# Optimization experiments

Hardware: AMD Instinct MI355X
Metric: run time of the kernel (lower is better)

The kernel has to match this reference:

```python
import jax, jax.numpy as jnp
import numpy as np

N_NODES = 100000
N_EDGES = 640000
D_IN = 128
D_OUT = 128


def setup_inputs() -> dict:
    key = jax.random.key(0)
    k1, k2, k3, k4 = jax.random.split(key, 4)
    x = jax.random.normal(k1, (N_NODES, D_IN), dtype=jnp.float32)
    edge_index = jax.random.randint(k2, (2, N_EDGES), 0, N_NODES, dtype=jnp.int64)
    # nn.Linear(input_dim, out_dim): weight [out, in], bias [out]
    bound = 1.0 / np.sqrt(D_IN)
    W = jax.random.uniform(k3, (D_OUT, D_IN), minval=-bound, maxval=bound, dtype=jnp.float32)
    b = jax.random.uniform(k4, (D_OUT,), minval=-bound, maxval=bound, dtype=jnp.float32)
    return {"x": x, "edge_index": edge_index, "W": W, "b": b}


def reference(x, edge_index, W, b):
    # GINConv (eps=0): h_i = (1+eps)*x_i + sum_{j in N(i)} x_j, then Linear(h)
    src = edge_index[0]
    dst = edge_index[1]
    agg = jax.ops.segment_sum(x[src], dst, num_segments=N_NODES)  # [N, D_IN]
    h = x + agg
    return h @ W.T + b  # [N, D_OUT]
```

## Files before the change

kernel.cpp:

```cpp
#include <hip/hip_runtime.h>
#include <hip/hip_bf16.h>

#define N_NODES 100000
#define N_EDGES 640000
#define D 128
#define NBINS 782
#define NBINSP 784
#define CHB 320
#define CHE 2000
#define CAP 2048
#define GB 1563
#define TB (GB + CHB)
#define ZROW N_NODES
#define CSRN (NBINS * 128)

typedef __attribute__((ext_vector_type(8))) short short8;
typedef __attribute__((ext_vector_type(4))) float f32x4;

__device__ __forceinline__ short f32_to_bf16(float f) {
  union { float f; unsigned u; } c; c.f = f;
  unsigned u = c.u;
  unsigned r = (u + 0x7FFFu + ((u >> 16) & 1u)) >> 16;
  return (short)r;
}
__device__ __forceinline__ float lo_bf16(unsigned v) {
  union { unsigned u; float f; } c; c.u = v << 16; return c.f;
}
__device__ __forceinline__ float hi_bf16(unsigned v) {
  union { unsigned u; float f; } c; c.u = v & 0xFFFF0000u; return c.f;
}

__global__ __launch_bounds__(256) void gemm_count(const float* x, const float* W,
                                                  const int* ei, short* y, int* hist) {
  __shared__ char ldsbuf[128 * 136 * 2];
  int b = blockIdx.x;
  int g_incl = ((b + 1) * GB) / TB;
  bool is_gemm = g_incl > (b * GB) / TB;
  int t = threadIdx.x;

  if (!is_gemm) {
    int* h = (int*)ldsbuf;
    int sid = b - g_incl;
    for (int j = t; j < NBINSP; j += 256) h[j] = 0;
    __syncthreads();
    int base = sid * CHE;
    for (int i = t; i < CHE; i += 256) {
      int dst = ei[N_EDGES + base + i];
      atomicAdd(&h[dst >> 7], 1);
    }
    __syncthreads();
    for (int j = t; j < NBINSP; j += 256) hist[sid * NBINSP + j] = h[j];
    return;
  }

  short (*Wlds)[136] = (short(*)[136])ldsbuf;
  int gb = g_incl - 1;
  for (int idx = t * 8; idx < D * D; idx += 256 * 8) {
    int r = idx >> 7, c = idx & 127;
    float4 a = *reinterpret_cast<const float4*>(W + idx);
    float4 bb = *reinterpret_cast<const float4*>(W + idx + 4);
    short8 s;
    s[0] = f32_to_bf16(a.x);  s[1] = f32_to_bf16(a.y);
    s[2] = f32_to_bf16(a.z);  s[3] = f32_to_bf16(a.w);
    s[4] = f32_to_bf16(bb.x); s[5] = f32_to_bf16(bb.y);
    s[6] = f32_to_bf16(bb.z); s[7] = f32_to_bf16(bb.w);
    *reinterpret_cast<short8*>(&Wlds[r][c]) = s;
  }
  __syncthreads();

  int wave = t >> 6, lane = t & 63;
  int l15 = lane & 15, kq = lane >> 4;
  int row0 = gb * 64 + wave * 16;
  if (row0 >= N_NODES) return;
  int ar = row0 + l15;
  if (ar >= N_NODES) ar = N_NODES - 1;
  const float* xrow = x + (size_t)ar * D;

  f32x4 acc[8];
#pragma unroll
  for (int n = 0; n < 8; ++n) acc[n] = (f32x4){0.f, 0.f, 0.f, 0.f};

#pragma unroll
  for (int kk = 0; kk < 4; ++kk) {
    int k0 = kk * 32 + kq * 8;
    float4 a0 = *reinterpret_cast<const float4*>(xrow + k0);
    float4 a1 = *reinterpret_cast<const float4*>(xrow + k0 + 4);
    short8 af;
    af[0] = f32_to_bf16(a0.x); af[1] = f32_to_bf16(a0.y);
    af[2] = f32_to_bf16(a0.z); af[3] = f32_to_bf16(a0.w);
    af[4] = f32_to_bf16(a1.x); af[5] = f32_to_bf16(a1.y);
    af[6] = f32_to_bf16(a1.z); af[7] = f32_to_bf16(a1.w);
#pragma unroll
    for (int n = 0; n < 8; ++n) {
      short8 bf = *reinterpret_cast<short8*>(&Wlds[n * 16 + l15][k0]);
      acc[n] = __builtin_amdgcn_mfma_f32_16x16x32_bf16(af, bf, acc[n], 0, 0, 0);
    }
  }

  int orow0 = row0 + kq * 4;
#pragma unroll
  for (int n = 0; n < 8; ++n) {
#pragma unroll
    for (int r = 0; r < 4; ++r) {
      int row = orow0 + r;
      if (row < N_NODES)
        y[(size_t)row * D + n * 16 + l15] = f32_to_bf16(acc[n][r]);
    }
  }
}

__global__ __launch_bounds__(256) void scan_cols(const int* hist, int* scanned, int* bintot) {
  __shared__ int sdata[256];
  int j = blockIdx.x;
  int t = threadIdx.x;
  int a = 0, b = 0;
  if (t < CHB / 2) {
    a = hist[(2 * t) * NBINSP + j];
    b = hist[(2 * t + 1) * NBINSP + j];
  }
  int ps = a + b;
  sdata[t] = ps;
  __syncthreads();
  int incl = ps;
  for (int off = 1; off < 256; off <<= 1) {
    int u = (t >= off) ? sdata[t - off] : 0;
    __syncthreads();
    incl += u;
    sdata[t] = incl;
    __syncthreads();
  }
  if (t < CHB / 2) {
    int excl = incl - ps;
    scanned[j * CHB + 2 * t] = excl;
    scanned[j * CHB + 2 * t + 1] = excl + a;
  }
  if (t == CHB / 2 - 1) bintot[j] = incl;
}

__global__ __launch_bounds__(256) void scan_bins(const int* bintot, int* bases, short* y) {
  __shared__ int sdata[256];
  int t = threadIdx.x;
  if (t < 64) ((int*)(y + (size_t)ZROW * D))[t] = 0;

  int v0 = 0, v1 = 0, v2 = 0, v3 = 0;
  if (t < NBINSP / 4) {
    int4 vv = *reinterpret_cast<const int4*>(bintot + 4 * t);
    v0 = vv.x; v1 = vv.y; v2 = vv.z; v3 = vv.w;
  }
  int s = v0 + v1 + v2 + v3;
  sdata[t] = s;
  __syncthreads();
  int incl = s;
  for (int off = 1; off < 256; off <<= 1) {
    int u = (t >= off) ? sdata[t - off] : 0;
    __syncthreads();
    incl += u;
    sdata[t] = incl;
    __syncthreads();
  }
  if (t < NBINSP / 4) {
    int e = incl - s;
    bases[4 * t + 0] = e;
    bases[4 * t + 1] = e + v0;
    bases[4 * t + 2] = e + v0 + v1;
    bases[4 * t + 3] = e + v0 + v1 + v2;
  }
  if (t == NBINSP / 4 - 1) bases[NBINSP] = incl;
}

__global__ __launch_bounds__(256) void bin_place(const int* ei, const int* scanned,
                                                 const int* bases, int* binned) {
  __shared__ int rk[NBINSP];
  __shared__ int cb[NBINSP];
  int t = threadIdx.x, b = blockIdx.x;
  for (int j = t; j < NBINSP; j += 256) {
    rk[j] = 0;
    cb[j] = bases[j] + scanned[j * CHB + b];
  }
  __syncthreads();
  int base = b * CHE;
  for (int i = t; i < CHE; i += 256) {
    int e = base + i;
    int src = ei[e];
    int dst = ei[N_EDGES + e];
    int bin = dst >> 7;
    int r = atomicAdd(&rk[bin], 1);
    binned[cb[bin] + r] = ((dst & 127) << 17) | src;
  }
}

__global__ __launch_bounds__(256) void sort_bins32(const int* binned, const int* bases,
                                                   int* csr32, int* ndeg) {
  __shared__ int c[128];
  int bin = blockIdx.x, t = threadIdx.x;
  if (t < 128) c[t] = 0;
  __syncthreads();
  int est = bases[bin];
  int E = bases[bin + 1] - est;
  if (E > CAP) E = CAP;

#pragma unroll
  for (int j = 0; j < 8; ++j) {
    int i = j * 256 + t;
    if (i < E) {
      int p = binned[est + i];
      int off = p >> 17;
      int r = atomicAdd(&c[off], 1);
      if (r < 32)
        csr32[(size_t)((bin << 7) + off) * 32 + r] = p & 0x1FFFF;
    }
  }
  __syncthreads();

  if (t < 128) {
    int gnode = (bin << 7) + t;
    if (gnode < N_NODES) ndeg[gnode] = c[t];
  }
  for (int s = t; s < 128 * 32; s += 256) {
    int node = s >> 5, slot = s & 31;
    if (slot >= c[node])
      csr32[(size_t)((bin << 7) + node) * 32 + slot] = ZROW;
  }
}

__global__ __launch_bounds__(256) void gather32(const short* y, const int* ndeg,
                                                const int* csr32, const float* bias,
                                                float* out) {
  int gtid = blockIdx.x * 256 + threadIdx.x;
  int wave = gtid >> 6;
  int lane = threadIdx.x & 63;
  int g = lane >> 5;
  int l = lane & 31;
  int node = wave * 2 + g;

  int deg = ndeg[node];
  if (deg > 32) deg = 32;
  int dother = __shfl_xor(deg, 32);
  int kmaxw = deg > dother ? deg : dother;

  int ids = csr32[(size_t)node * 32 + l];
  int base_sl = lane & 32;

  const uint2* yq = (const uint2*)y;
  uint2 self = yq[(size_t)node * 32 + l];

  float4 acc[8];
#pragma unroll
  for (int i = 0; i < 8; ++i) acc[i] = make_float4(0.f, 0.f, 0.f, 0.f);

  for (int k = 0; k < kmaxw; k += 8) {
#pragma unroll
    for (int i = 0; i < 8; ++i) {
      int src = __shfl(ids, base_sl + k + i);
      uint2 w = yq[(size_t)src * 32 + l];
      acc[i].x += lo_bf16(w.x);
      acc[i].y += hi_bf16(w.x);
      acc[i].z += lo_bf16(w.y);
      acc[i].w += hi_bf16(w.y);
    }
  }

  float4 bv = ((const float4*)bias)[l];
  float4 tot;
  tot.x = (lo_bf16(self.x) + bv.x) + (((acc[0].x + acc[1].x) + (acc[2].x + acc[3].x)) +
                                      ((acc[4].x + acc[5].x) + (acc[6].x + acc[7].x)));
  tot.y = (hi_bf16(self.x) + bv.y) + (((acc[0].y + acc[1].y) + (acc[2].y + acc[3].y)) +
                                      ((acc[4].y + acc[5].y) + (acc[6].y + acc[7].y)));
  tot.z = (lo_bf16(self.y) + bv.z) + (((acc[0].z + acc[1].z) + (acc[2].z + acc[3].z)) +
                                      ((acc[4].z + acc[5].z) + (acc[6].z + acc[7].z)));
  tot.w = (hi_bf16(self.y) + bv.w) + (((acc[0].w + acc[1].w) + (acc[2].w + acc[3].w)) +
                                      ((acc[4].w + acc[5].w) + (acc[6].w + acc[7].w)));

  ((float4*)out)[(size_t)node * 32 + l] = tot;
}

__global__ void copy_x(const float4* x, float4* h, int n4) {
  int i = blockIdx.x * blockDim.x + threadIdx.x;
  int s = gridDim.x * blockDim.x;
  for (; i < n4; i += s) h[i] = x[i];
}

__global__ void scatter_add(const float* x, const int* ei, float* h) {
  int i = blockIdx.x * blockDim.x + threadIdx.x;
  int s = gridDim.x * blockDim.x;
  const int total = N_EDGES * 32;
  for (; i < total; i += s) {
    int e = i >> 5;
    int c = (i & 31) << 2;
    int src = ei[e];
    int dst = ei[N_EDGES + e];
    float4 v = *reinterpret_cast<const float4*>(x + (size_t)src * D + c);
    float* hp = h + (size_t)dst * D + c;
    unsafeAtomicAdd(hp + 0, v.x);
    unsafeAtomicAdd(hp + 1, v.y);
    unsafeAtomicAdd(hp + 2, v.z);
    unsafeAtomicAdd(hp + 3, v.w);
  }
}

__global__ __launch_bounds__(256) void gin_gemm_f32(const float* h, const float* W,
                                                    const float* bias, float* out) {
  __shared__ short Wlds[128][136];
  int t = threadIdx.x;
  for (int idx = t * 8; idx < D * D; idx += 256 * 8) {
    int r = idx >> 7, c = idx & 127;
    float4 a = *reinterpret_cast<const float4*>(W + idx);
    float4 b = *reinterpret_cast<const float4*>(W + idx + 4);
    short8 s;
    s[0] = f32_to_bf16(a.x); s[1] = f32_to_bf16(a.y);
    s[2] = f32_to_bf16(a.z); s[3] = f32_to_bf16(a.w);
    s[4] = f32_to_bf16(b.x); s[5] = f32_to_bf16(b.y);
    s[6] = f32_to_bf16(b.z); s[7] = f32_to_bf16(b.w);
    *reinterpret_cast<short8*>(&Wlds[r][c]) = s;
  }
  __syncthreads();

  int wave = t >> 6, lane = t & 63;
  int l15 = lane & 15, kq = lane >> 4;
  int row0 = blockIdx.x * 64 + wave * 16;
  if (row0 >= N_NODES) return;
  int ar = row0 + l15;
  if (ar >= N_NODES) ar = N_NODES - 1;
  const float* hrow = h + (size_t)ar * D;

  f32x4 acc[8];
#pragma unroll
  for (int n = 0; n < 8; ++n) acc[n] = (f32x4){0.f, 0.f, 0.f, 0.f};

#pragma unroll
  for (int kk = 0; kk < 4; ++kk) {
    int k0 = kk * 32 + kq * 8;
    float4 a0 = *reinterpret_cast<const float4*>(hrow + k0);
    float4 a1 = *reinterpret_cast<const float4*>(hrow + k0 + 4);
    short8 af;
    af[0] = f32_to_bf16(a0.x); af[1] = f32_to_bf16(a0.y);
    af[2] = f32_to_bf16(a0.z); af[3] = f32_to_bf16(a0.w);
    af[4] = f32_to_bf16(a1.x); af[5] = f32_to_bf16(a1.y);
    af[6] = f32_to_bf16(a1.z); af[7] = f32_to_bf16(a1.w);
#pragma unroll
    for (int n = 0; n < 8; ++n) {
      short8 bf = *reinterpret_cast<short8*>(&Wlds[n * 16 + l15][k0]);
      acc[n] = __builtin_amdgcn_mfma_f32_16x16x32_bf16(af, bf, acc[n], 0, 0, 0);
    }
  }

  int orow0 = row0 + kq * 4;
#pragma unroll
  for (int n = 0; n < 8; ++n) {
    float bv = bias[n * 16 + l15];
#pragma unroll
    for (int r = 0; r < 4; ++r) {
      int row = orow0 + r;
      if (row < N_NODES)
        out[(size_t)row * D + n * 16 + l15] = acc[n][r] + bv;
    }
  }
}

extern "C" void kernel_launch(void* const* d_in, const int* in_sizes, int n_in,
                              void* d_out, int out_size, void* d_ws, size_t ws_size,
                              hipStream_t stream) {
  const float* x   = (const float*)d_in[0];
  const int*   ei  = (const int*)d_in[1];
  const float* W   = (const float*)d_in[2];
  const float* bia = (const float*)d_in[3];
  float* out = (float*)d_out;
  (void)in_sizes; (void)n_in; (void)out_size;

  const size_t HIST_I   = (size_t)CHB * NBINSP;
  const size_t SCAN_I   = (size_t)NBINSP * CHB;
  const size_t BINTOT_I = NBINSP;
  const size_t BASES_I  = 800;
  const size_t BINNED_I = N_EDGES;
  const size_t CSR_I    = (size_t)CSRN * 32;
  const size_t NDG_I    = CSRN;
  const size_t INTS = HIST_I + SCAN_I + BINTOT_I + BASES_I + BINNED_I + CSR_I + NDG_I;
  const size_t Y_B  = (size_t)(N_NODES + 1) * D * 2;
  const size_t NEED = INTS * 4 + Y_B;

  if (ws_size >= NEED) {
    int* hist    = (int*)d_ws;
    int* scanned = hist + HIST_I;
    int* bintot  = scanned + SCAN_I;
    int* bases   = bintot + BINTOT_I;
    int* binned  = bases + BASES_I;
    int* csr32   = binned + BINNED_I;
    int* ndeg    = csr32 + CSR_I;
    short* y     = (short*)(ndeg + NDG_I);

    gemm_count <<<TB, 256, 0, stream>>>(x, W, ei, y, hist);
    scan_cols  <<<NBINSP, 256, 0, stream>>>(hist, scanned, bintot);
    scan_bins  <<<1, 256, 0, stream>>>(bintot, bases, y);
    bin_place  <<<CHB, 256, 0, stream>>>(ei, scanned, bases, binned);
    sort_bins32<<<NBINS, 256, 0, stream>>>(binned, bases, csr32, ndeg);
    gather32   <<<(N_NODES / 2) / 4, 256, 0, stream>>>(y, ndeg, csr32, bia, out);
  } else {
    int n4 = N_NODES * D / 4;
    copy_x<<<(n4 + 255) / 256, 256, 0, stream>>>((const float4*)x, (float4*)out, n4);
    int total = N_EDGES * 32;
    scatter_add<<<(total + 255) / 256, 256, 0, stream>>>(x, ei, out);
    gin_gemm_f32<<<(N_NODES + 63) / 64, 256, 0, stream>>>(out, W, bia, out);
  }
}
```

Before: 92.17 us.

## Split GEMM across place and sort kernels, use nontemporal memory ops

```diff
diff --git a/kernel.cpp b/kernel.cpp
--- a/kernel.cpp
+++ b/kernel.cpp
@@ -9,8 +9,9 @@
 #define CHB 320
 #define CHE 2000
 #define CAP 2048
-#define GB 1563
-#define TB (GB + CHB)
+#define GBT 1563
+#define GA 400
+#define GB2 (GBT - GA)
 #define ZROW N_NODES
 #define CSRN (NBINS * 128)
 
@@ -30,31 +31,10 @@
   union { unsigned u; float f; } c; c.u = v & 0xFFFF0000u; return c.f;
 }
 
-__global__ __launch_bounds__(256) void gemm_count(const float* x, const float* W,
-                                                  const int* ei, short* y, int* hist) {
-  __shared__ char ldsbuf[128 * 136 * 2];
-  int b = blockIdx.x;
-  int g_incl = ((b + 1) * GB) / TB;
-  bool is_gemm = g_incl > (b * GB) / TB;
-  int t = threadIdx.x;
-
-  if (!is_gemm) {
-    int* h = (int*)ldsbuf;
-    int sid = b - g_incl;
-    for (int j = t; j < NBINSP; j += 256) h[j] = 0;
-    __syncthreads();
-    int base = sid * CHE;
-    for (int i = t; i < CHE; i += 256) {
-      int dst = ei[N_EDGES + base + i];
-      atomicAdd(&h[dst >> 7], 1);
-    }
-    __syncthreads();
-    for (int j = t; j < NBINSP; j += 256) hist[sid * NBINSP + j] = h[j];
-    return;
-  }
-
+__device__ __forceinline__ void gemm_body(const float* x, const float* W, short* y,
+                                          int gb, char* ldsbuf) {
   short (*Wlds)[136] = (short(*)[136])ldsbuf;
-  int gb = g_incl - 1;
+  int t = threadIdx.x;
   for (int idx = t * 8; idx < D * D; idx += 256 * 8) {
     int r = idx >> 7, c = idx & 127;
     float4 a = *reinterpret_cast<const float4*>(W + idx);
@@ -109,6 +89,27 @@
   }
 }
 
+#define HETERO_MAP(S_, G_)                                   \
+  int b = blockIdx.x;                                        \
+  int g_incl = ((b + 1) * (G_)) / ((S_) + (G_));             \
+  bool is_gemm = g_incl > (b * (G_)) / ((S_) + (G_));        \
+  int sid = b - g_incl;                                      \
+  int gb_loc = g_incl - 1;
+
+__global__ __launch_bounds__(256) void bin_count(const int* ei, int* hist) {
+  __shared__ int h[NBINSP];
+  int t = threadIdx.x, b = blockIdx.x;
+  for (int j = t; j < NBINSP; j += 256) h[j] = 0;
+  __syncthreads();
+  int base = b * CHE;
+  for (int i = t; i < CHE; i += 256) {
+    int dst = ei[N_EDGES + base + i];
+    atomicAdd(&h[dst >> 7], 1);
+  }
+  __syncthreads();
+  for (int j = t; j < NBINSP; j += 256) hist[b * NBINSP + j] = h[j];
+}
+
 __global__ __launch_bounds__(256) void scan_cols(const int* hist, int* scanned, int* bintot) {
   __shared__ int sdata[256];
   int j = blockIdx.x;
@@ -168,31 +169,44 @@
   if (t == NBINSP / 4 - 1) bases[NBINSP] = incl;
 }
 
-__global__ __launch_bounds__(256) void bin_place(const int* ei, const int* scanned,
-                                                 const int* bases, int* binned) {
-  __shared__ int rk[NBINSP];
-  __shared__ int cb[NBINSP];
-  int t = threadIdx.x, b = blockIdx.x;
+__global__ __launch_bounds__(256) void p4_place_gemm(const float* x, const float* W,
+                                                     short* y, const int* ei,
+                                                     const int* scanned, const int* bases,
+                                                     int* binned) {
+  __shared__ char ldsbuf[34816];
+  HETERO_MAP(CHB, GA)
+  int t = threadIdx.x;
+  if (is_gemm) { gemm_body(x, W, y, gb_loc, ldsbuf); return; }
+
+  int* rk = (int*)ldsbuf;
+  int* cb = rk + NBINSP;
   for (int j = t; j < NBINSP; j += 256) {
     rk[j] = 0;
-    cb[j] = bases[j] + scanned[j * CHB + b];
-  }
-  __syncthreads();
-  int base = b * CHE;
+    cb[j] = bases[j] + scanned[j * CHB + sid];
+  }
+  __syncthreads();
+  int base = sid * CHE;
   for (int i = t; i < CHE; i += 256) {
     int e = base + i;
     int src = ei[e];
     int dst = ei[N_EDGES + e];
     int bin = dst >> 7;
     int r = atomicAdd(&rk[bin], 1);
-    binned[cb[bin] + r] = ((dst & 127) << 17) | src;
-  }
-}
-
-__global__ __launch_bounds__(256) void sort_bins32(const int* binned, const int* bases,
-                                                   int* csr32, int* ndeg) {
-  __shared__ int c[128];
-  int bin = blockIdx.x, t = threadIdx.x;
+    __builtin_nontemporal_store(((dst & 127) << 17) | src, &binned[cb[bin] + r]);
+  }
+}
+
+__global__ __launch_bounds__(256) void p5_sort_gemm(const float* x, const float* W,
+                                                    short* y, const int* binned,
+                                                    const int* bases, int* csr32,
+                                                    int* ndeg) {
+  __shared__ char ldsbuf[34816];
+  HETERO_MAP(NBINS, GB2)
+  int t = threadIdx.x;
+  if (is_gemm) { gemm_body(x, W, y, GA + gb_loc, ldsbuf); return; }
+
+  int* c = (int*)ldsbuf;
+  int bin = sid;
   if (t < 128) c[t] = 0;
   __syncthreads();
   int est = bases[bin];
@@ -203,11 +217,12 @@
   for (int j = 0; j < 8; ++j) {
     int i = j * 256 + t;
     if (i < E) {
-      int p = binned[est + i];
+      int p = __builtin_nontemporal_load(&binned[est + i]);
       int off = p >> 17;
       int r = atomicAdd(&c[off], 1);
       if (r < 32)
-        csr32[(size_t)((bin << 7) + off) * 32 + r] = p & 0x1FFFF;
+        __builtin_nontemporal_store(p & 0x1FFFF,
+            &csr32[(size_t)((bin << 7) + off) * 32 + r]);
     }
   }
   __syncthreads();
@@ -219,7 +234,8 @@
   for (int s = t; s < 128 * 32; s += 256) {
     int node = s >> 5, slot = s & 31;
     if (slot >= c[node])
-      csr32[(size_t)((bin << 7) + node) * 32 + slot] = ZROW;
+      __builtin_nontemporal_store(ZROW,
+          &csr32[(size_t)((bin << 7) + node) * 32 + slot]);
   }
 }
 
@@ -233,12 +249,12 @@
   int l = lane & 31;
   int node = wave * 2 + g;
 
-  int deg = ndeg[node];
+  int deg = __builtin_nontemporal_load(&ndeg[node]);
   if (deg > 32) deg = 32;
   int dother = __shfl_xor(deg, 32);
   int kmaxw = deg > dother ? deg : dother;
 
-  int ids = csr32[(size_t)node * 32 + l];
+  int ids = __builtin_nontemporal_load(&csr32[(size_t)node * 32 + l]);
   int base_sl = lane & 32;
 
   const uint2* yq = (const uint2*)y;
@@ -261,17 +277,17 @@
   }
 
   float4 bv = ((const float4*)bias)[l];
-  float4 tot;
-  tot.x = (lo_bf16(self.x) + bv.x) + (((acc[0].x + acc[1].x) + (acc[2].x + acc[3].x)) +
-                                      ((acc[4].x + acc[5].x) + (acc[6].x + acc[7].x)));
-  tot.y = (hi_bf16(self.x) + bv.y) + (((acc[0].y + acc[1].y) + (acc[2].y + acc[3].y)) +
-                                      ((acc[4].y + acc[5].y) + (acc[6].y + acc[7].y)));
-  tot.z = (lo_bf16(self.y) + bv.z) + (((acc[0].z + acc[1].z) + (acc[2].z + acc[3].z)) +
-                                      ((acc[4].z + acc[5].z) + (acc[6].z + acc[7].z)));
-  tot.w = (hi_bf16(self.y) + bv.w) + (((acc[0].w + acc[1].w) + (acc[2].w + acc[3].w)) +
-                                      ((acc[4].w + acc[5].w) + (acc[6].w + acc[7].w)));
-
-  ((float4*)out)[(size_t)node * 32 + l] = tot;
+  f32x4 tot;
+  tot[0] = (lo_bf16(self.x) + bv.x) + (((acc[0].x + acc[1].x) + (acc[2].x + acc[3].x)) +
+                                       ((acc[4].x + acc[5].x) + (acc[6].x + acc[7].x)));
+  tot[1] = (hi_bf16(self.x) + bv.y) + (((acc[0].y + acc[1].y) + (acc[2].y + acc[3].y)) +
+                                       ((acc[4].y + acc[5].y) + (acc[6].y + acc[7].y)));
+  tot[2] = (lo_bf16(self.y) + bv.z) + (((acc[0].z + acc[1].z) + (acc[2].z + acc[3].z)) +
+                                       ((acc[4].z + acc[5].z) + (acc[6].z + acc[7].z)));
+  tot[3] = (hi_bf16(self.y) + bv.w) + (((acc[0].w + acc[1].w) + (acc[2].w + acc[3].w)) +
+                                       ((acc[4].w + acc[5].w) + (acc[6].w + acc[7].w)));
+
+  __builtin_nontemporal_store(tot, (f32x4*)out + (size_t)node * 32 + l);
 }
 
 __global__ void copy_x(const float4* x, float4* h, int n4) {
@@ -388,12 +404,12 @@
     int* ndeg    = csr32 + CSR_I;
     short* y     = (short*)(ndeg + NDG_I);
 
-    gemm_count <<<TB, 256, 0, stream>>>(x, W, ei, y, hist);
-    scan_cols  <<<NBINSP, 256, 0, stream>>>(hist, scanned, bintot);
-    scan_bins  <<<1, 256, 0, stream>>>(bintot, bases, y);
-    bin_place  <<<CHB, 256, 0, stream>>>(ei, scanned, bases, binned);
-    sort_bins32<<<NBINS, 256, 0, stream>>>(binned, bases, csr32, ndeg);
-    gather32   <<<(N_NODES / 2) / 4, 256, 0, stream>>>(y, ndeg, csr32, bia, out);
+    bin_count   <<<CHB, 256, 0, stream>>>(ei, hist);
+    scan_cols   <<<NBINSP, 256, 0, stream>>>(hist, scanned, bintot);
+    scan_bins   <<<1, 256, 0, stream>>>(bintot, bases, y);
+    p4_place_gemm<<<CHB + GA, 256, 0, stream>>>(x, W, y, ei, scanned, bases, binned);
+    p5_sort_gemm <<<NBINS + GB2, 256, 0, stream>>>(x, W, y, binned, bases, csr32, ndeg);
+    gather32    <<<(N_NODES / 2) / 4, 256, 0, stream>>>(y, ndeg, csr32, bia, out);
   } else {
     int n4 = N_NODES * D / 4;
     copy_x<<<(n4 + 255) / 256, 256, 0, stream>>>((const float4*)x, (float4*)out, n4);
```

Result: slower. 105.3 us (+14.2%).
